# Kernel tuning notes

Measured on AMD Instinct MI355X. Metric: run time of the kernel, lower is better.

Reference implementation:

```python
import jax, jax.numpy as jnp
import numpy as np

N, E, C_IN, C_OUT = 50000, 800000, 64, 64
BN_EPS = 1e-5


def _batchnorm(h, gamma, beta):
    # Training-mode BatchNorm1d: batch statistics over dim 0, biased variance.
    mean = h.mean(axis=0)
    var = h.var(axis=0)  # ddof=0, matches PyTorch normalization stats
    return gamma * (h - mean) * jax.lax.rsqrt(var + BN_EPS) + beta


def setup_inputs() -> dict:
    key = jax.random.key(0)
    ks = jax.random.split(key, 6)
    x = jax.random.normal(ks[0], (N, C_IN), dtype=jnp.float32)
    edge_index = jax.random.randint(ks[1], (2, E), 0, N, dtype=jnp.int32)
    edge_weight = jax.random.uniform(ks[2], (E,), dtype=jnp.float32)
    s1 = 1.0 / np.sqrt(C_IN).astype(np.float32)
    s2 = 1.0 / np.sqrt(2 * C_IN).astype(np.float32)
    pool_W = jax.random.uniform(ks[3], (C_IN, C_IN), jnp.float32, -s1, s1)
    pool_b = jnp.zeros((C_IN,), jnp.float32)
    final_W = jax.random.uniform(ks[4], (2 * C_IN, C_OUT), jnp.float32, -s2, s2)
    final_b = jnp.zeros((C_OUT,), jnp.float32)
    return {
        "x": x,
        "edge_index": edge_index,
        "edge_weight": edge_weight,
        "pool_W": pool_W,
        "pool_b": pool_b,
        "bn_pool_gamma": jnp.ones((C_IN,), jnp.float32),
        "bn_pool_beta": jnp.zeros((C_IN,), jnp.float32),
        "final_W": final_W,
        "final_b": final_b,
        "bn_final_gamma": jnp.ones((C_OUT,), jnp.float32),
        "bn_final_beta": jnp.zeros((C_OUT,), jnp.float32),
        "coef": jnp.float32(0.5),
    }


def reference(x, edge_index, edge_weight, pool_W, pool_b, bn_pool_gamma,
              bn_pool_beta, final_W, final_b, bn_final_gamma, bn_final_beta,
              coef):
    src, dst = edge_index[0], edge_index[1]
    # gather src node features, scale by edge weight  -> [E, C_IN]
    edge_feat = x[src] * (1.0 + coef * edge_weight[:, None])
    pooled = edge_feat @ pool_W + pool_b              # [E, C_IN]
    pooled = jax.nn.relu(_batchnorm(pooled, bn_pool_gamma, bn_pool_beta))
    # scatter-max into destination nodes; empty segments -> 0 (pooled >= 0)
    agg = jax.ops.segment_max(pooled, dst, num_segments=x.shape[0])
    agg = jnp.maximum(agg, 0.0)                       # fill -inf (empty) with 0
    h = jnp.concatenate([x, agg], axis=-1) @ final_W + final_b  # [N, C_OUT]
    h = _batchnorm(h, bn_final_gamma, bn_final_beta)
    return jax.nn.relu(h)
```

## Files before the change

kernel.cpp:

```cpp
#include <hip/hip_runtime.h>
#include <hip/hip_fp16.h>
#include <math.h>
#include <float.h>

#define BN_EPS 1e-5f
#define SLOTS 64


typedef __attribute__((ext_vector_type(8))) short bf16x8;
typedef __attribute__((ext_vector_type(4))) float f32x4;

__device__ inline unsigned short f2bf(float f) {
    unsigned u = __float_as_uint(f);
    return (unsigned short)((u + 0x7fffu + ((u >> 16) & 1u)) >> 16);
}
__device__ inline float bf2f(unsigned short h) {
    return __uint_as_float(((unsigned)h) << 16);
}

__global__ __launch_bounds__(256, 4) void k_scatter_pool(
        const int* __restrict__ src, const int* __restrict__ dst,
        const float* __restrict__ w, const float* __restrict__ coef_p,
        int* __restrict__ cnt, unsigned* __restrict__ csr, int E,
        const float* __restrict__ x, const float* __restrict__ W,
        unsigned short* __restrict__ ybf, int nrows, int SB) {
    __shared__ unsigned short Wt[64 * 72];
    if ((int)blockIdx.x < SB) {
        const int p = blockIdx.x & 7;
        const int q = blockIdx.x >> 3;
        const int SBq = SB >> 3;
        const int Npart = (nrows + 7) >> 3;
        const int lo = p * Npart;
        const int hi = (lo + Npart < nrows) ? lo + Npart : nrows;
        const float coef = *coef_p;
        for (int i = q * 256 + threadIdx.x; i < E; i += SBq * 256) {
            int tn = dst[i];
            if (tn >= lo && tn < hi) {
                int sn = src[i];
                float s = fmaf(coef, w[i], 1.0f);
                unsigned hs = (unsigned)__half_as_ushort(__float2half(s));
                int pos = atomicAdd(&cnt[tn], 1);
                if (pos < SLOTS)
                    csr[(size_t)tn * SLOTS + pos] = ((unsigned)sn << 16) | hs;
            }
        }
        return;
    }
    for (int i = threadIdx.x; i < 64 * 64; i += 256) {
        int k = i >> 6, n = i & 63;
        Wt[n * 72 + k] = f2bf(W[i]);
    }
    __syncthreads();
    const int lane = threadIdx.x & 63;
    const int wave = threadIdx.x >> 6;
    const int quad = lane >> 4;
    const int ln = lane & 15;
    bf16x8 Bf[2][4];
#pragma unroll
    for (int kc = 0; kc < 2; ++kc)
#pragma unroll
        for (int ct = 0; ct < 4; ++ct)
            Bf[kc][ct] = *(const bf16x8*)&Wt[(ct * 16 + ln) * 72 + kc * 32 + quad * 8];
    const int T = (nrows + 15) >> 4;
    const int gw = ((int)blockIdx.x - SB) * 4 + wave;
    const int nw = ((int)gridDim.x - SB) * 4;
    for (int t = gw; t < T; t += nw) {
        const int row = t * 16 + ln;
        bf16x8 af[2];
        if (row < nrows) {
            const float* xr = x + (size_t)row * 64;
#pragma unroll
            for (int kc = 0; kc < 2; ++kc) {
                float4 pv = *(const float4*)(xr + kc * 32 + quad * 8);
                float4 qv = *(const float4*)(xr + kc * 32 + quad * 8 + 4);
                bf16x8 a;
                a[0] = (short)f2bf(pv.x); a[1] = (short)f2bf(pv.y);
                a[2] = (short)f2bf(pv.z); a[3] = (short)f2bf(pv.w);
                a[4] = (short)f2bf(qv.x); a[5] = (short)f2bf(qv.y);
                a[6] = (short)f2bf(qv.z); a[7] = (short)f2bf(qv.w);
                af[kc] = a;
            }
        } else {
            bf16x8 z;
#pragma unroll
            for (int j = 0; j < 8; ++j) z[j] = 0;
            af[0] = z; af[1] = z;
        }
        f32x4 acc[4];
#pragma unroll
        for (int ct = 0; ct < 4; ++ct) { acc[ct][0]=0.f; acc[ct][1]=0.f; acc[ct][2]=0.f; acc[ct][3]=0.f; }
#pragma unroll
        for (int ct = 0; ct < 4; ++ct) {
            acc[ct] = __builtin_amdgcn_mfma_f32_16x16x32_bf16(af[0], Bf[0][ct], acc[ct], 0, 0, 0);
            acc[ct] = __builtin_amdgcn_mfma_f32_16x16x32_bf16(af[1], Bf[1][ct], acc[ct], 0, 0, 0);
        }
#pragma unroll
        for (int r = 0; r < 4; ++r) {
            int ro = t * 16 + quad * 4 + r;
            if (ro < nrows) {
#pragma unroll
                for (int ct = 0; ct < 4; ++ct)
                    ybf[(size_t)ro * 64 + ct * 16 + ln] = f2bf(acc[ct][r]);
            }
        }
    }
}

__global__ __launch_bounds__(256) void k_gather_max(const unsigned short* __restrict__ ybf,
                             const unsigned* __restrict__ csr, const int* __restrict__ cnt,
                             float* __restrict__ M, float* __restrict__ partials, int nrows) {
    int sub = threadIdx.x & 15;
    int rg = threadIdx.x >> 4;
    int c0 = sub * 4;
    float s1[4] = {0, 0, 0, 0}, s2[4] = {0, 0, 0, 0};
    const int nchunks = (nrows + 15) >> 4;
    for (int nb = blockIdx.x; nb < nchunks; nb += gridDim.x) {
        int node = nb * 16 + rg;
        size_t base = (size_t)node * SLOTS;
        int dg = 0;
        if (node < nrows) { dg = cnt[node]; if (dg > SLOTS) dg = SLOTS; }
        float m0 = -FLT_MAX, m1 = -FLT_MAX, m2 = -FLT_MAX, m3 = -FLT_MAX;
        for (int k0 = 0; k0 < dg; k0 += 16) {
            int kk = k0 + sub;
            unsigned pk = (kk < dg) ? csr[base + kk] : 0u;
            int cnt16 = dg - k0; if (cnt16 > 16) cnt16 = 16;
            for (int j = 0; j < cnt16; ++j) {
                unsigned r = (unsigned)__shfl((int)pk, j, 16);
                int sn = r >> 16;
                float sv = __half2float(__ushort_as_half((unsigned short)(r & 0xffffu)));
                ushort4 uv = *(const ushort4*)&ybf[(size_t)sn * 64 + c0];
                float v0 = sv * bf2f(uv.x), v1 = sv * bf2f(uv.y);
                float v2 = sv * bf2f(uv.z), v3 = sv * bf2f(uv.w);
                m0 = fmaxf(m0, v0); s1[0] += v0; s2[0] = fmaf(v0, v0, s2[0]);
                m1 = fmaxf(m1, v1); s1[1] += v1; s2[1] = fmaf(v1, v1, s2[1]);
                m2 = fmaxf(m2, v2); s1[2] += v2; s2[2] = fmaf(v2, v2, s2[2]);
                m3 = fmaxf(m3, v3); s1[3] += v3; s2[3] = fmaf(v3, v3, s2[3]);
            }
        }
        if (node < nrows)
            *(float4*)&M[(size_t)node * 64 + c0] = make_float4(m0, m1, m2, m3);
    }
    __shared__ float red[16][68];
#pragma unroll
    for (int j = 0; j < 4; ++j) red[rg][c0 + j] = s1[j];
    __syncthreads();
    if (rg == 0) {
#pragma unroll
        for (int j = 0; j < 4; ++j) {
            float tt = 0.0f;
            for (int r = 0; r < 16; ++r) tt += red[r][c0 + j];
            partials[(size_t)blockIdx.x * 128 + c0 + j] = tt;
        }
    }
    __syncthreads();
#pragma unroll
    for (int j = 0; j < 4; ++j) red[rg][c0 + j] = s2[j];
    __syncthreads();
    if (rg == 0) {
#pragma unroll
        for (int j = 0; j < 4; ++j) {
            float tt = 0.0f;
            for (int r = 0; r < 16; ++r) tt += red[r][c0 + j];
            partials[(size_t)blockIdx.x * 128 + 64 + c0 + j] = tt;
        }
    }
}

__global__ __launch_bounds__(256) void k_red1(const float* __restrict__ partials, int P,
                                              float* __restrict__ p2) {
    int c = threadIdx.x & 127;
    int half = threadIdx.x >> 7;
    float acc = 0.0f;
    for (int r = blockIdx.x * 2 + half; r < P; r += 256)
        acc += partials[(size_t)r * 128 + c];
    __shared__ float sh[256];
    sh[threadIdx.x] = acc;
    __syncthreads();
    if (half == 0) p2[(size_t)blockIdx.x * 128 + c] = sh[c] + sh[128 + c];
}

__global__ __launch_bounds__(1024) void k_red2(const float* __restrict__ p2,
                             const float* __restrict__ pool_b, const float* __restrict__ gamma,
                             const float* __restrict__ beta, float invE,
                             float* __restrict__ coef) {
    int c = threadIdx.x & 127;
    int seg = threadIdx.x >> 7;
    float acc = 0.0f;
    for (int r = seg; r < 128; r += 8) acc += p2[(size_t)r * 128 + c];
    __shared__ float red[8][128];
    red[seg][c] = acc;
    __syncthreads();
    if (seg == 0) {
        float tt = 0.0f;
#pragma unroll
        for (int s = 0; s < 8; ++s) tt += red[s][c];
        red[0][c] = tt;
    }
    __syncthreads();
    if (threadIdx.x < 64) {
        int c0 = threadIdx.x;
        float S1 = red[0][c0], S2 = red[0][64 + c0];
        float s1 = S1 * invE;
        float b = pool_b[c0];
        float mean = s1 + b;
        float ex2 = S2 * invE + 2.0f * b * s1 + b * b;
        float var = ex2 - mean * mean;
        float a = gamma[c0] * rsqrtf(var + BN_EPS);
        coef[c0] = a;
        coef[64 + c0] = beta[c0] - a * s1;
    }
}

__global__ __launch_bounds__(1024) void k_red2f(const float* __restrict__ p2,
                             const float* __restrict__ gamma, const float* __restrict__ beta,
                             float invN, float* __restrict__ coef) {
    int c = threadIdx.x & 127;
    int seg = threadIdx.x >> 7;
    float acc = 0.0f;
    for (int r = seg; r < 128; r += 8) acc += p2[(size_t)r * 128 + c];
    __shared__ float red[8][128];
    red[seg][c] = acc;
    __syncthreads();
    if (seg == 0) {
        float tt = 0.0f;
#pragma unroll
        for (int s = 0; s < 8; ++s) tt += red[s][c];
        red[0][c] = tt;
    }
    __syncthreads();
    if (threadIdx.x < 64) {
        int c0 = threadIdx.x;
        float mean = red[0][c0] * invN;
        float var = red[0][64 + c0] * invN - mean * mean;
        float a = gamma[c0] * rsqrtf(var + BN_EPS);
        coef[c0] = a;
        coef[64 + c0] = beta[c0] - a * mean;
    }
}

__global__ __launch_bounds__(256, 2) void k_final_gemm(const float* __restrict__ x,
                             const float* __restrict__ M, const float* __restrict__ coef,
                             const float* __restrict__ W, const float* __restrict__ b,
                             float* __restrict__ h, float* __restrict__ partials, int nrows) {
    __shared__ unsigned short Wt[64 * 136];
    __shared__ float hp[128];
    for (int i = threadIdx.x; i < 128 * 64; i += 256) {
        int k = i >> 6, n = i & 63;
        Wt[n * 136 + k] = f2bf(W[i]);
    }
    if (threadIdx.x < 128) hp[threadIdx.x] = 0.0f;
    __syncthreads();
    const int lane = threadIdx.x & 63;
    const int wave = threadIdx.x >> 6;
    const int quad = lane >> 4;
    const int ln = lane & 15;
    bf16x8 Bf[4][4];
#pragma unroll
    for (int kc = 0; kc < 4; ++kc)
#pragma unroll
        for (int ct = 0; ct < 4; ++ct)
            Bf[kc][ct] = *(const bf16x8*)&Wt[(ct * 16 + ln) * 136 + kc * 32 + quad * 8];
    float bias[4];
#pragma unroll
    for (int ct = 0; ct < 4; ++ct) bias[ct] = b[ct * 16 + ln];
    float ca[2][8], cd[2][8];
#pragma unroll
    for (int g = 0; g < 2; ++g) {
        int ch = g * 32 + quad * 8;
#pragma unroll
        for (int j = 0; j < 8; ++j) {
            ca[g][j] = coef[ch + j];
            cd[g][j] = coef[64 + ch + j];
        }
    }
    float ls1[4] = {0, 0, 0, 0}, ls2[4] = {0, 0, 0, 0};
    const int T = (nrows + 15) >> 4;
    const int gw = blockIdx.x * 4 + wave;
    const int nw = gridDim.x * 4;
    for (int t = gw; t < T; t += nw) {
        const int row = t * 16 + ln;
        bf16x8 af[4];
        if (row < nrows) {
            const float* xr = x + (size_t)row * 64;
#pragma unroll
            for (int kc = 0; kc < 2; ++kc) {
                float4 pv = *(const float4*)(xr + kc * 32 + quad * 8);
                float4 qv = *(const float4*)(xr + kc * 32 + quad * 8 + 4);
                bf16x8 a;
                a[0] = (short)f2bf(pv.x); a[1] = (short)f2bf(pv.y);
                a[2] = (short)f2bf(pv.z); a[3] = (short)f2bf(pv.w);
                a[4] = (short)f2bf(qv.x); a[5] = (short)f2bf(qv.y);
                a[6] = (short)f2bf(qv.z); a[7] = (short)f2bf(qv.w);
                af[kc] = a;
            }
            const float* mr = M + (size_t)row * 64;
#pragma unroll
            for (int g = 0; g < 2; ++g) {
                const float* mp = mr + g * 32 + quad * 8;
                float4 pv = *(const float4*)mp;
                float4 qv = *(const float4*)(mp + 4);
                float v[8] = {pv.x, pv.y, pv.z, pv.w, qv.x, qv.y, qv.z, qv.w};
                bf16x8 a;
#pragma unroll
                for (int j = 0; j < 8; ++j)
                    a[j] = (short)f2bf(fmaxf(fmaf(ca[g][j], v[j], cd[g][j]), 0.0f));
                af[2 + g] = a;
            }
        } else {
            bf16x8 z;
#pragma unroll
            for (int j = 0; j < 8; ++j) z[j] = 0;
#pragma unroll
            for (int kc = 0; kc < 4; ++kc) af[kc] = z;
        }
        f32x4 acc[4];
#pragma unroll
        for (int ct = 0; ct < 4; ++ct) { acc[ct][0]=0.f; acc[ct][1]=0.f; acc[ct][2]=0.f; acc[ct][3]=0.f; }
#pragma unroll
        for (int kc = 0; kc < 4; ++kc)
#pragma unroll
            for (int ct = 0; ct < 4; ++ct)
                acc[ct] = __builtin_amdgcn_mfma_f32_16x16x32_bf16(af[kc], Bf[kc][ct], acc[ct], 0, 0, 0);
#pragma unroll
        for (int r = 0; r < 4; ++r) {
            int ro = t * 16 + quad * 4 + r;
            if (ro < nrows) {
#pragma unroll
                for (int ct = 0; ct < 4; ++ct) {
                    float hv = acc[ct][r] + bias[ct];
                    h[(size_t)ro * 64 + ct * 16 + ln] = hv;
                    ls1[ct] += hv;
                    ls2[ct] = fmaf(hv, hv, ls2[ct]);
                }
            }
        }
    }
#pragma unroll
    for (int ct = 0; ct < 4; ++ct) {
        atomicAdd(&hp[ct * 16 + ln], ls1[ct]);
        atomicAdd(&hp[64 + ct * 16 + ln], ls2[ct]);
    }
    __syncthreads();
    if (threadIdx.x < 128)
        partials[(size_t)blockIdx.x * 128 + threadIdx.x] = hp[threadIdx.x];
}

__global__ __launch_bounds__(256) void k_bn_out(const float* __restrict__ h,
                         const float* __restrict__ coef,
                         float* __restrict__ out, int nrows) {
    const int idx = blockIdx.x * blockDim.x + threadIdx.x;
    const int total = nrows * 16;
    if (idx >= total) return;
    const int c0 = (idx & 15) * 4;
    const float4 hv = *(const float4*)(h + (size_t)idx * 4);
    float4 o;
    float* op = (float*)&o;
    const float* hp = (const float*)&hv;
#pragma unroll
    for (int j = 0; j < 4; ++j) {
        const int c = c0 + j;
        op[j] = fmaxf(fmaf(coef[c], hp[j], coef[64 + c]), 0.0f);
    }
    *(float4*)(out + (size_t)idx * 4) = o;
}

extern "C" void kernel_launch(void* const* d_in, const int* in_sizes, int n_in,
                              void* d_out, int out_size, void* d_ws, size_t ws_size,
                              hipStream_t stream) {
    const float* x       = (const float*)d_in[0];
    const int*   eidx    = (const int*)d_in[1];
    const float* ew      = (const float*)d_in[2];
    const float* pool_W  = (const float*)d_in[3];
    const float* pool_b  = (const float*)d_in[4];
    const float* g1      = (const float*)d_in[5];
    const float* b1      = (const float*)d_in[6];
    const float* final_W = (const float*)d_in[7];
    const float* final_b = (const float*)d_in[8];
    const float* g2      = (const float*)d_in[9];
    const float* b2      = (const float*)d_in[10];
    const float* coef    = (const float*)d_in[11];

    const int N = in_sizes[0] / 64;
    const int E = in_sizes[1] / 2;
    const int* src = eidx;
    const int* dst = eidx + E;

    const int SB  = 2048;
    const int T   = (N + 15) / 16;
    const int nbT = (T + 3) / 4;
    const int PG  = 1024;

    unsigned* ws = (unsigned*)d_ws;
    int*   cnt      = (int*)ws;
    float* bncoef   = (float*)(ws + (size_t)N);
    float* coef2    = (float*)(ws + (size_t)N + 128);
    float* p2       = (float*)(ws + (size_t)N + 256);
    float* p2F      = p2 + 16384;
    float* partialsG= p2F + 16384;
    float* partialsF= partialsG + (size_t)PG * 128;
    unsigned short* ybf = (unsigned short*)(partialsF + (size_t)nbT * 128);
    unsigned* csrF  = (unsigned*)ybf + (size_t)32 * N;
    float* M        = (float*)(csrF + (size_t)SLOTS * N);

    hipMemsetAsync(cnt, 0, (size_t)N * 4, stream);

    k_scatter_pool<<<SB + nbT, 256, 0, stream>>>(src, dst, ew, coef, cnt, csrF, E,
                                                 x, pool_W, ybf, N, SB);
    k_gather_max<<<PG, 256, 0, stream>>>(ybf, csrF, cnt, M, partialsG, N);
    k_red1   <<<128, 256, 0, stream>>>(partialsG, PG, p2);
    k_red2   <<<1, 1024, 0, stream>>>(p2, pool_b, g1, b1, 1.0f / (float)E, bncoef);
    k_final_gemm<<<nbT, 256, 0, stream>>>(x, M, bncoef, final_W, final_b,
                                          (float*)d_out, partialsF, N);
    k_red1   <<<128, 256, 0, stream>>>(partialsF, nbT, p2F);
    k_red2f  <<<1, 1024, 0, stream>>>(p2F, g2, b2, 1.0f / (float)N, coef2);
    k_bn_out <<<(N * 16 + 255) / 256, 256, 0, stream>>>((const float*)d_out, coef2,
                                                        (float*)d_out, N);
}
```

Before: 218.7 us.

## Replace partial-sum reduction kernels with atomics and drop dst-range scatter partitioning

The gather-max and final GEMM kernels now atomically add their per-block BN statistics into 128 pre-zeroed rows, so both k_red1 launches are removed and k_red2 reads those rows directly. One memset now clears the counts and both accumulation buffers. The scatter phase no longer splits destinations into 8 node ranges that each rescan all edges; every edge is processed once, with the scatter block count raised from 2048 to 3072. This saves two launches and seven redundant passes over the edge arrays, in exchange for float atomic contention, atomic-order nondeterminism, and less locality in the count/CSR writes.

```diff
diff --git a/kernel.cpp b/kernel.cpp
--- a/kernel.cpp
+++ b/kernel.cpp
@@ -26,23 +26,15 @@
         unsigned short* __restrict__ ybf, int nrows, int SB) {
     __shared__ unsigned short Wt[64 * 72];
     if ((int)blockIdx.x < SB) {
-        const int p = blockIdx.x & 7;
-        const int q = blockIdx.x >> 3;
-        const int SBq = SB >> 3;
-        const int Npart = (nrows + 7) >> 3;
-        const int lo = p * Npart;
-        const int hi = (lo + Npart < nrows) ? lo + Npart : nrows;
         const float coef = *coef_p;
-        for (int i = q * 256 + threadIdx.x; i < E; i += SBq * 256) {
+        for (int i = blockIdx.x * 256 + threadIdx.x; i < E; i += SB * 256) {
             int tn = dst[i];
-            if (tn >= lo && tn < hi) {
-                int sn = src[i];
-                float s = fmaf(coef, w[i], 1.0f);
-                unsigned hs = (unsigned)__half_as_ushort(__float2half(s));
-                int pos = atomicAdd(&cnt[tn], 1);
-                if (pos < SLOTS)
-                    csr[(size_t)tn * SLOTS + pos] = ((unsigned)sn << 16) | hs;
-            }
+            int sn = src[i];
+            float s = fmaf(coef, w[i], 1.0f);
+            unsigned hs = (unsigned)__half_as_ushort(__float2half(s));
+            int pos = atomicAdd(&cnt[tn], 1);
+            if (pos < SLOTS)
+                csr[(size_t)tn * SLOTS + pos] = ((unsigned)sn << 16) | hs;
         }
         return;
     }
@@ -108,7 +100,7 @@
 
 __global__ __launch_bounds__(256) void k_gather_max(const unsigned short* __restrict__ ybf,
                              const unsigned* __restrict__ csr, const int* __restrict__ cnt,
-                             float* __restrict__ M, float* __restrict__ partials, int nrows) {
+                             float* __restrict__ M, float* __restrict__ pG2, int nrows) {
     int sub = threadIdx.x & 15;
     int rg = threadIdx.x >> 4;
     int c0 = sub * 4;
@@ -141,6 +133,7 @@
             *(float4*)&M[(size_t)node * 64 + c0] = make_float4(m0, m1, m2, m3);
     }
     __shared__ float red[16][68];
+    float* prow = pG2 + (size_t)(blockIdx.x & 127) * 128;
 #pragma unroll
     for (int j = 0; j < 4; ++j) red[rg][c0 + j] = s1[j];
     __syncthreads();
@@ -149,7 +142,7 @@
         for (int j = 0; j < 4; ++j) {
             float tt = 0.0f;
             for (int r = 0; r < 16; ++r) tt += red[r][c0 + j];
-            partials[(size_t)blockIdx.x * 128 + c0 + j] = tt;
+            atomicAdd(&prow[c0 + j], tt);
         }
     }
     __syncthreads();
@@ -161,22 +154,9 @@
         for (int j = 0; j < 4; ++j) {
             float tt = 0.0f;
             for (int r = 0; r < 16; ++r) tt += red[r][c0 + j];
-            partials[(size_t)blockIdx.x * 128 + 64 + c0 + j] = tt;
-        }
-    }
-}
-
-__global__ __launch_bounds__(256) void k_red1(const float* __restrict__ partials, int P,
-                                              float* __restrict__ p2) {
-    int c = threadIdx.x & 127;
-    int half = threadIdx.x >> 7;
-    float acc = 0.0f;
-    for (int r = blockIdx.x * 2 + half; r < P; r += 256)
-        acc += partials[(size_t)r * 128 + c];
-    __shared__ float sh[256];
-    sh[threadIdx.x] = acc;
-    __syncthreads();
-    if (half == 0) p2[(size_t)blockIdx.x * 128 + c] = sh[c] + sh[128 + c];
+            atomicAdd(&prow[64 + c0 + j], tt);
+        }
+    }
 }
 
 __global__ __launch_bounds__(1024) void k_red2(const float* __restrict__ p2,
@@ -241,7 +221,7 @@
 __global__ __launch_bounds__(256, 2) void k_final_gemm(const float* __restrict__ x,
                              const float* __restrict__ M, const float* __restrict__ coef,
                              const float* __restrict__ W, const float* __restrict__ b,
-                             float* __restrict__ h, float* __restrict__ partials, int nrows) {
+                             float* __restrict__ h, float* __restrict__ pF2, int nrows) {
     __shared__ unsigned short Wt[64 * 136];
     __shared__ float hp[128];
     for (int i = threadIdx.x; i < 128 * 64; i += 256) {
@@ -342,7 +322,7 @@
     }
     __syncthreads();
     if (threadIdx.x < 128)
-        partials[(size_t)blockIdx.x * 128 + threadIdx.x] = hp[threadIdx.x];
+        atomicAdd(&pF2[(size_t)(blockIdx.x & 127) * 128 + threadIdx.x], hp[threadIdx.x]);
 }
 
 __global__ __launch_bounds__(256) void k_bn_out(const float* __restrict__ h,
@@ -385,34 +365,30 @@
     const int* src = eidx;
     const int* dst = eidx + E;
 
-    const int SB  = 2048;
+    const int SB  = 3072;
     const int T   = (N + 15) / 16;
     const int nbT = (T + 3) / 4;
     const int PG  = 1024;
 
     unsigned* ws = (unsigned*)d_ws;
-    int*   cnt      = (int*)ws;
-    float* bncoef   = (float*)(ws + (size_t)N);
-    float* coef2    = (float*)(ws + (size_t)N + 128);
-    float* p2       = (float*)(ws + (size_t)N + 256);
-    float* p2F      = p2 + 16384;
-    float* partialsG= p2F + 16384;
-    float* partialsF= partialsG + (size_t)PG * 128;
-    unsigned short* ybf = (unsigned short*)(partialsF + (size_t)nbT * 128);
-    unsigned* csrF  = (unsigned*)ybf + (size_t)32 * N;
-    float* M        = (float*)(csrF + (size_t)SLOTS * N);
-
-    hipMemsetAsync(cnt, 0, (size_t)N * 4, stream);
-
-    k_scatter_pool<<<SB + nbT, 256, 0, stream>>>(src, dst, ew, coef, cnt, csrF, E,
+    int*   cnt    = (int*)ws;
+    float* pG2    = (float*)(ws + (size_t)N);
+    float* pF2    = (float*)(ws + (size_t)N + 16384);
+    float* bncoef = (float*)(ws + (size_t)N + 32768);
+    float* coef2  = (float*)(ws + (size_t)N + 32896);
+    unsigned short* ybf = (unsigned short*)(ws + (size_t)N + 33024);
+    unsigned* csr = ws + (size_t)N + 33024 + (size_t)32 * N;
+    float* M      = (float*)(csr + (size_t)SLOTS * N);
+
+    hipMemsetAsync(d_ws, 0, ((size_t)N + 32768) * 4, stream);
+
+    k_scatter_pool<<<SB + nbT, 256, 0, stream>>>(src, dst, ew, coef, cnt, csr, E,
                                                  x, pool_W, ybf, N, SB);
-    k_gather_max<<<PG, 256, 0, stream>>>(ybf, csrF, cnt, M, partialsG, N);
-    k_red1   <<<128, 256, 0, stream>>>(partialsG, PG, p2);
-    k_red2   <<<1, 1024, 0, stream>>>(p2, pool_b, g1, b1, 1.0f / (float)E, bncoef);
+    k_gather_max<<<PG, 256, 0, stream>>>(ybf, csr, cnt, M, pG2, N);
+    k_red2   <<<1, 1024, 0, stream>>>(pG2, pool_b, g1, b1, 1.0f / (float)E, bncoef);
     k_final_gemm<<<nbT, 256, 0, stream>>>(x, M, bncoef, final_W, final_b,
-                                          (float*)d_out, partialsF, N);
-    k_red1   <<<128, 256, 0, stream>>>(partialsF, nbT, p2F);
-    k_red2f  <<<1, 1024, 0, stream>>>(p2F, g2, b2, 1.0f / (float)N, coef2);
+                                          (float*)d_out, pF2, N);
+    k_red2f  <<<1, 1024, 0, stream>>>(pF2, g2, b2, 1.0f / (float)N, coef2);
     k_bn_out <<<(N * 16 + 255) / 256, 256, 0, stream>>>((const float*)d_out, coef2,
                                                         (float*)d_out, N);
 }
```

Result: no change. 221.9 us (+1.5%).
